# Kernel tuning notes

Measured on AMD Instinct MI355X. Metric: run time of the kernel, lower is better.

## Reference

```python
import jax, jax.numpy as jnp
import numpy as np

T, B, D, H = 2048, 4, 1024, 16
DK = D // H
SCALE = 1.0 / np.sqrt(DK)


def setup_inputs() -> dict:
    key = jax.random.key(0)
    k1, k2, k3 = jax.random.split(key, 3)
    x = jax.random.normal(k1, (T, B, D), dtype=jnp.float32)
    # xavier_uniform-ish scaling
    W_qkv = jax.random.normal(k2, (3 * D, D), dtype=jnp.float32) * np.sqrt(2.0 / (D + 3 * D))
    W_out = jax.random.normal(k3, (D, D), dtype=jnp.float32) * np.sqrt(1.0 / D)
    b_out = jnp.zeros((D,), dtype=jnp.float32)
    return {"x": x, "W_qkv": W_qkv, "W_out": W_out, "b_out": b_out}


def reference(x, W_qkv, W_out, b_out):
    Tn, Bn, Dn = x.shape
    # QKV projection (Linear with weight [3D, D], no bias)
    qkv = x @ W_qkv.T                                  # (T, B, 3D)
    qkv = qkv.reshape(Tn, Bn, 3, H, DK)
    q, k, v = qkv[:, :, 0], qkv[:, :, 1], qkv[:, :, 2]  # each (T, B, H, dk)
    scores = jnp.einsum('tbhd,sbhd->bhts', q, k) * SCALE  # (B, H, T, T)
    causal = jnp.triu(jnp.ones((Tn, Tn), dtype=bool), k=1)
    scores = jnp.where(causal, -jnp.inf, scores)
    attn = jax.nn.softmax(scores, axis=-1)
    out = jnp.einsum('bhts,sbhd->tbhd', attn, v)        # (T, B, H, dk)
    out = out.reshape(Tn, Bn, Dn)
    return out @ W_out.T + b_out
```

## Files before the change

### kernel.cpp

```cpp
#include <hip/hip_runtime.h>
#include <stdint.h>

#define T_DIM 2048
#define B_DIM 4
#define D_DIM 1024
#define H_NUM 16
#define HD 64
#define MROWS (T_DIM * B_DIM)
#define QKV_N (3 * D_DIM)
#define ATT_C 0.18033688011112042f

typedef unsigned short u16;
typedef __bf16 bf16x8 __attribute__((ext_vector_type(8)));
typedef float f32x4 __attribute__((ext_vector_type(4)));
typedef float f32x16 __attribute__((ext_vector_type(16)));
typedef u16 u16x4 __attribute__((ext_vector_type(4)));
typedef u16 u16x8 __attribute__((ext_vector_type(8)));

__device__ __forceinline__ u16 f2bf(float f) {
  union { float f; unsigned u; } v; v.f = f;
  unsigned r = v.u + 0x7fffu + ((v.u >> 16) & 1u);
  return (u16)(r >> 16);
}

__device__ __forceinline__ void async_copy16(void* lds, const void* g) {
  __builtin_amdgcn_global_load_lds((__attribute__((address_space(1))) void*)(g),
                                   (__attribute__((address_space(3))) void*)(lds),
                                   16, 0, 0);
}

__global__ __launch_bounds__(256) void cast3_f32_bf16(
    const float* __restrict__ s0, const float* __restrict__ s1,
    const float* __restrict__ s2, u16* __restrict__ dst,
    int n0, int n01, int ntot4) {
  int i = blockIdx.x * 256 + threadIdx.x;
  if (i >= ntot4) return;
  int e = i * 4;
  const float* s; int off;
  if (e < n0) { s = s0; off = 0; }
  else if (e < n01) { s = s1; off = n0; }
  else { s = s2; off = n01; }
  float4 v = *reinterpret_cast<const float4*>(s + (e - off));
  u16x4 o = {f2bf(v.x), f2bf(v.y), f2bf(v.z), f2bf(v.w)};
  *reinterpret_cast<u16x4*>(dst + e) = o;
}

template <int OUT_F32_BIAS>
__global__ __launch_bounds__(512, 1) void gemm_bt8b(
    const u16* __restrict__ A, const u16* __restrict__ Bm,
    u16* __restrict__ Cb, float* __restrict__ Cf, const float* __restrict__ bias,
    int M, int N, int K) {
  extern __shared__ u16 sm[];

  const int tid = threadIdx.x;
  const int lane = tid & 63, wid = tid >> 6;
  const int wr = wid >> 2, wc = wid & 3;
  const int l15 = lane & 15, lg = lane >> 4;
  const int xr = ((l15 >> 2) & 1) << 4;

  const int nwg = gridDim.x * gridDim.y;
  const int lin = blockIdx.y * gridDim.x + blockIdx.x;
  const int swz = (lin & 7) * (nwg >> 3) + (lin >> 3);
  const int bx = swz % gridDim.x, by = swz / gridDim.x;
  const int m0 = by * 128, n0 = bx * 256;

  const int srow = tid >> 3;
  const int kxs = ((tid & 7) * 8) ^ (((tid >> 5) & 1) << 4);
  const u16* gA = A + (size_t)(m0 + srow) * K + kxs;
  const u16* gB = Bm + (size_t)(n0 + srow) * K + kxs;

#define STGA(tk_, c_)                                                           \
  {                                                                             \
    _Pragma("unroll") for (int p = 0; p < 2; ++p)                               \
      async_copy16(sm + (c_) * 24576 + p * 4096 + tid * 8,                      \
                   gA + (size_t)(p * 64) * K + (size_t)(tk_) * 64);             \
  }
#define STGB(tk_, c_)                                                           \
  {                                                                             \
    _Pragma("unroll") for (int p = 0; p < 4; ++p)                               \
      async_copy16(sm + (c_) * 24576 + 8192 + p * 4096 + tid * 8,               \
                   gB + (size_t)(p * 64) * K + (size_t)(tk_) * 64);             \
  }
#define LDA_(mt_, kk_, c_)                                                      \
  (*reinterpret_cast<const bf16x8*>(sm + (c_) * 24576 +                         \
      (wr * 64 + (mt_) * 16 + l15) * 64 + (((kk_) * 32 + lg * 8) ^ xr)))
#define LDB_(nt_, kk_, c_)                                                      \
  (*reinterpret_cast<const bf16x8*>(sm + (c_) * 24576 + 8192 +                  \
      (wc * 64 + (nt_) * 16 + l15) * 64 + (((kk_) * 32 + lg * 8) ^ xr)))

  f32x4 acc[4][4];
#pragma unroll
  for (int i = 0; i < 4; i++)
#pragma unroll
    for (int j = 0; j < 4; j++) acc[i][j] = (f32x4){0.f, 0.f, 0.f, 0.f};

  const int NT = K >> 6;

  STGA(0, 0) STGB(0, 0) STGA(1, 1)
  asm volatile("s_waitcnt vmcnt(2)" ::: "memory");
  __builtin_amdgcn_sched_barrier(0);
  __builtin_amdgcn_s_barrier();

  for (int t = 0; t < NT; ++t) {
    const int c = t & 1;
    bf16x8 a03[4][2], b01[2][2], b23[2][2];
#pragma unroll
    for (int mt = 0; mt < 4; ++mt) {
      a03[mt][0] = LDA_(mt, 0, c);
      a03[mt][1] = LDA_(mt, 1, c);
    }
#pragma unroll
    for (int nt = 0; nt < 2; ++nt) {
      b01[nt][0] = LDB_(nt, 0, c);
      b01[nt][1] = LDB_(nt, 1, c);
    }
    if (t + 1 < NT) STGB(t + 1, c ^ 1)
    __builtin_amdgcn_s_barrier();
    asm volatile("s_waitcnt lgkmcnt(0)" ::: "memory");
    __builtin_amdgcn_sched_barrier(0);
    __builtin_amdgcn_s_setprio(1);
#pragma unroll
    for (int mt = 0; mt < 4; ++mt)
#pragma unroll
      for (int nt = 0; nt < 2; ++nt)
#pragma unroll
        for (int kk = 0; kk < 2; ++kk)
          acc[mt][nt] = __builtin_amdgcn_mfma_f32_16x16x32_bf16(
              a03[mt][kk], b01[nt][kk], acc[mt][nt], 0, 0, 0);
    __builtin_amdgcn_s_setprio(0);
    __builtin_amdgcn_s_barrier();
#pragma unroll
    for (int nt = 0; nt < 2; ++nt) {
      b23[nt][0] = LDB_(nt + 2, 0, c);
      b23[nt][1] = LDB_(nt + 2, 1, c);
    }
    if (t + 2 < NT) STGA(t + 2, c)
    __builtin_amdgcn_s_barrier();
    asm volatile("s_waitcnt lgkmcnt(0)" ::: "memory");
    __builtin_amdgcn_sched_barrier(0);
    __builtin_amdgcn_s_setprio(1);
#pragma unroll
    for (int mt = 0; mt < 4; ++mt)
#pragma unroll
      for (int nt = 0; nt < 2; ++nt)
#pragma unroll
        for (int kk = 0; kk < 2; ++kk)
          acc[mt][nt + 2] = __builtin_amdgcn_mfma_f32_16x16x32_bf16(
              a03[mt][kk], b23[nt][kk], acc[mt][nt + 2], 0, 0, 0);
    __builtin_amdgcn_s_setprio(0);
    if (t + 1 < NT) {
      if (t + 2 < NT) {
        asm volatile("s_waitcnt vmcnt(2)" ::: "memory");
      } else {
        asm volatile("s_waitcnt vmcnt(0)" ::: "memory");
      }
      __builtin_amdgcn_sched_barrier(0);
    }
    __builtin_amdgcn_s_barrier();
  }

  const float qsc = (!OUT_F32_BIAS && n0 < D_DIM) ? ATT_C : 1.0f;
#pragma unroll
  for (int mt = 0; mt < 4; ++mt) {
#pragma unroll
    for (int r = 0; r < 4; ++r) {
      const int row = m0 + wr * 64 + mt * 16 + lg * 4 + r;
#pragma unroll
      for (int nt = 0; nt < 4; ++nt) {
        const int col = n0 + wc * 64 + nt * 16 + l15;
        if (OUT_F32_BIAS) {
          Cf[(size_t)row * N + col] = acc[mt][nt][r] + bias[col];
        } else {
          Cb[(size_t)row * N + col] = f2bf(acc[mt][nt][r] * qsc);
        }
      }
    }
  }
#undef STGA
#undef STGB
#undef LDA_
#undef LDB_
}

#define VF_STRIDE 24
#define VF_FRAG (32 * VF_STRIDE)

__device__ __forceinline__ void process32(
    const bf16x8 (&qf)[4], f32x16 (&o)[2], f32x16& lacc,
    int q0w, int kv0, int l31, int hi, bool needMask, const bf16x8 onesf,
    const u16* __restrict__ Ks, const u16* __restrict__ Vf) {
  f32x16 s[2];
#pragma unroll
  for (int kb = 0; kb < 2; ++kb)
#pragma unroll
    for (int r = 0; r < 16; ++r) s[kb][r] = 0.f;

  __builtin_amdgcn_s_setprio(1);
#pragma unroll
  for (int kb = 0; kb < 2; ++kb) {
#pragma unroll
    for (int ks = 0; ks < 4; ++ks) {
      const int row = kb * 32 + l31;
      bf16x8 kf = *reinterpret_cast<const bf16x8*>(
          &Ks[row * 64 + ((((ks << 1) | hi)) ^ (l31 & 7)) * 8]);
      s[kb] = __builtin_amdgcn_mfma_f32_32x32x16_bf16(kf, qf[ks], s[kb], 0, 0, 0);
    }
  }
  __builtin_amdgcn_s_setprio(0);

  if (needMask) {
    const int q = q0w + l31;
#pragma unroll
    for (int kb = 0; kb < 2; ++kb)
#pragma unroll
      for (int r = 0; r < 16; ++r) {
        const int kv = kv0 + kb * 32 + (r & 3) + ((r >> 2) << 3) + (hi << 2);
        if (kv > q) s[kb][r] = -1e30f;
      }
  }
#pragma unroll
  for (int kb = 0; kb < 2; ++kb)
#pragma unroll
    for (int r = 0; r < 16; ++r)
      s[kb][r] = __builtin_amdgcn_exp2f(s[kb][r]);

  union Frag { unsigned u[4]; bf16x8 v; };
  Frag pf[4];
#pragma unroll
  for (int kb = 0; kb < 2; ++kb)
#pragma unroll
    for (int g = 0; g < 2; ++g) {
#pragma unroll
      for (int t2 = 0; t2 < 2; ++t2) {
        unsigned x, y;
        asm("v_cvt_pk_bf16_f32 %0, %1, %2"
            : "=v"(x) : "v"(s[kb][g * 8 + t2 * 2]), "v"(s[kb][g * 8 + t2 * 2 + 1]));
        asm("v_cvt_pk_bf16_f32 %0, %1, %2"
            : "=v"(y) : "v"(s[kb][g * 8 + t2 * 2 + 4]), "v"(s[kb][g * 8 + t2 * 2 + 5]));
        asm("v_permlane32_swap_b32 %0, %1" : "+v"(x), "+v"(y));
        pf[kb * 2 + g].u[t2] = x;
        pf[kb * 2 + g].u[t2 + 2] = y;
      }
    }

  __builtin_amdgcn_s_setprio(1);
#pragma unroll
  for (int ks = 0; ks < 4; ++ks) {
    lacc = __builtin_amdgcn_mfma_f32_32x32x16_bf16(onesf, pf[ks].v, lacc, 0, 0, 0);
#pragma unroll
    for (int db = 0; db < 2; ++db) {
      bf16x8 vf = *reinterpret_cast<const bf16x8*>(
          &Vf[(ks * 2 + db) * VF_FRAG + l31 * VF_STRIDE + hi * 8]);
      o[db] = __builtin_amdgcn_mfma_f32_32x32x16_bf16(vf, pf[ks].v, o[db], 0, 0, 0);
    }
  }
  __builtin_amdgcn_s_setprio(0);
}

__global__ __launch_bounds__(256, 2) void attn_kernel(
    const u16* __restrict__ qkv, u16* __restrict__ aout) {
  __shared__ __attribute__((aligned(16))) u16 Ks[128 * 64];
  __shared__ __attribute__((aligned(16))) u16 Vf[16 * VF_FRAG];

  const int tid = threadIdx.x;
  const int lane = tid & 63, w = tid >> 6;
  const int l31 = lane & 31, hi = lane >> 5;

  const int nwg = gridDim.x * gridDim.y;
  const int lin = blockIdx.y * gridDim.x + blockIdx.x;
  const int swz = (lin & 7) * (nwg >> 3) + (lin >> 3);
  const int px = swz % gridDim.x;
  const int bh = swz / gridDim.x;
  const int b = bh >> 4, h = bh & 15;
  const int qtA = px, qtB = 15 - px;
  const int q0A = qtA * 128 + w * 32, q0B = qtB * 128 + w * 32;

  bf16x8 qfA[4], qfB[4];
  {
    const u16* pA = qkv + ((size_t)(q0A + l31) * B_DIM + b) * QKV_N + h * HD + hi * 8;
    const u16* pB = qkv + ((size_t)(q0B + l31) * B_DIM + b) * QKV_N + h * HD + hi * 8;
#pragma unroll
    for (int ks = 0; ks < 4; ++ks) {
      qfA[ks] = *reinterpret_cast<const bf16x8*>(pA + ks * 16);
      qfB[ks] = *reinterpret_cast<const bf16x8*>(pB + ks * 16);
    }
  }

  bf16x8 onesf;
  {
    union { u16 u[8]; bf16x8 v; } ou;
#pragma unroll
    for (int i = 0; i < 8; ++i) ou.u[i] = 0x3F80;
    onesf = ou.v;
  }

  f32x16 oA[2], oB[2], laccA, laccB;
#pragma unroll
  for (int r = 0; r < 16; ++r) { laccA[r] = 0.f; laccB[r] = 0.f; }
#pragma unroll
  for (int db = 0; db < 2; ++db)
#pragma unroll
    for (int r = 0; r < 16; ++r) { oA[db][r] = 0.f; oB[db][r] = 0.f; }

  const int srow = tid >> 3;
  const int scol = (tid & 7) * 8;
  const int csw = (tid & 7) ^ (srow & 7);

  for (int kt2 = 0; kt2 <= qtB; ++kt2) {
    const int base = kt2 * 128;
#pragma unroll
    for (int p = 0; p < 4; ++p) {
      const u16* gK = qkv + ((size_t)(base + p * 32 + srow) * B_DIM + b) * QKV_N +
                      D_DIM + h * HD + csw * 8;
      async_copy16(Ks + tid * 8 + p * 2048, gK);
    }
    u16x8 vv[4];
#pragma unroll
    for (int p = 0; p < 4; ++p) {
      const u16* gV = qkv + ((size_t)(base + p * 32 + srow) * B_DIM + b) * QKV_N +
                      2 * D_DIM + h * HD + scol;
      vv[p] = *reinterpret_cast<const u16x8*>(gV);
    }
#pragma unroll
    for (int p = 0; p < 4; ++p) {
      const int kvl = p * 32 + srow;
      const int fb = (kvl >> 4) * 2;
      const int e16 = kvl & 15;
#pragma unroll
      for (int jj = 0; jj < 8; ++jj) {
        const int j = (jj + srow) & 7;
        const int d = scol + j;
        Vf[(fb + (d >> 5)) * VF_FRAG + (d & 31) * VF_STRIDE + e16] = vv[p][j];
      }
    }
    __syncthreads();

#pragma unroll
    for (int half = 0; half < 2; ++half) {
      const int kv0 = base + half * 64;
      const u16* Kh = Ks + half * (64 * 64);
      const u16* Vh = Vf + half * 8 * VF_FRAG;
      if (kv0 <= q0A + 31)
        process32(qfA, oA, laccA, q0A, kv0, l31, hi, kv0 + 63 > q0A, onesf, Kh, Vh);
      if (kv0 <= q0B + 31)
        process32(qfB, oB, laccB, q0B, kv0, l31, hi, kv0 + 63 > q0B, onesf, Kh, Vh);
    }
    __syncthreads();
  }

#pragma unroll
  for (int t = 0; t < 2; ++t) {
    const float inv = 1.0f / (t == 0 ? laccA[0] : laccB[0]);
    const int q0w = t == 0 ? q0A : q0B;
    f32x16* o = t == 0 ? oA : oB;
    u16* orow = aout + ((size_t)(q0w + l31) * B_DIM + b) * D_DIM + h * HD;
#pragma unroll
    for (int db = 0; db < 2; ++db)
#pragma unroll
      for (int rq = 0; rq < 4; ++rq) {
        u16x4 o4;
#pragma unroll
        for (int e = 0; e < 4; ++e) o4[e] = f2bf(o[db][rq * 4 + e] * inv);
        *reinterpret_cast<u16x4*>(orow + db * 32 + rq * 8 + hi * 4) = o4;
      }
  }
}

extern "C" void kernel_launch(void* const* d_in, const int* in_sizes, int n_in,
                              void* d_out, int out_size, void* d_ws, size_t ws_size,
                              hipStream_t stream) {
  (void)in_sizes; (void)n_in; (void)out_size; (void)ws_size;
  const float* x = (const float*)d_in[0];
  const float* Wqkv = (const float*)d_in[1];
  const float* Wout = (const float*)d_in[2];
  const float* bout = (const float*)d_in[3];
  float* out = (float*)d_out;

  u16* xb = (u16*)d_ws;
  u16* wqkvb = xb + (size_t)MROWS * D_DIM;
  u16* woutb = wqkvb + (size_t)QKV_N * D_DIM;
  u16* qkv = woutb + (size_t)D_DIM * D_DIM;
  u16* aout = qkv + (size_t)MROWS * QKV_N;

  {
    const int n0 = MROWS * D_DIM;
    const int n01 = n0 + QKV_N * D_DIM;
    const int ntot = n01 + D_DIM * D_DIM;
    const int n4 = ntot / 4;
    cast3_f32_bf16<<<(n4 + 255) / 256, 256, 0, stream>>>(
        x, Wqkv, Wout, xb, n0, n01, n4);
  }

  hipFuncSetAttribute((const void*)gemm_bt8b<0>,
                      hipFuncAttributeMaxDynamicSharedMemorySize, 98304);
  gemm_bt8b<0><<<dim3(QKV_N / 256, MROWS / 128), 512, 98304, stream>>>(
      xb, wqkvb, qkv, nullptr, nullptr, MROWS, QKV_N, D_DIM);

  attn_kernel<<<dim3(8, B_DIM * H_NUM), 256, 0, stream>>>(qkv, aout);

  hipFuncSetAttribute((const void*)gemm_bt8b<1>,
                      hipFuncAttributeMaxDynamicSharedMemorySize, 98304);
  gemm_bt8b<1><<<dim3(D_DIM / 256, MROWS / 128), 512, 98304, stream>>>(
      aout, woutb, nullptr, out, bout, MROWS, D_DIM, D_DIM);
}
```

Before: 178.5 us.

## Load V tiles via async global-to-LDS copy and read with transposing LDS loads

V tiles were loaded into registers and scattered element-by-element into a padded transposed LDS layout. Now they are copied straight to LDS with async global_load_lds in a blocked layout, and the MFMA operands are formed with ds_read_b64_tr_b16 transposing reads. This removes the register round trip and many 2-byte LDS stores per tile. In exchange it inserts a full lgkmcnt(0) wait and a sched_barrier before each set of PV MFMAs, which can serialize LDS latency with compute.

New measurement: 158.7 us, median of 2. 11.1% less time.

```diff
diff --git a/kernel.cpp b/kernel.cpp
--- a/kernel.cpp
+++ b/kernel.cpp
@@ -16,6 +16,7 @@
 typedef float f32x16 __attribute__((ext_vector_type(16)));
 typedef u16 u16x4 __attribute__((ext_vector_type(4)));
 typedef u16 u16x8 __attribute__((ext_vector_type(8)));
+typedef unsigned u32x2 __attribute__((ext_vector_type(2)));
 
 __device__ __forceinline__ u16 f2bf(float f) {
   union { float f; unsigned u; } v; v.f = f;
@@ -182,13 +183,11 @@
 #undef LDB_
 }
 
-#define VF_STRIDE 24
-#define VF_FRAG (32 * VF_STRIDE)
 
 __device__ __forceinline__ void process32(
     const bf16x8 (&qf)[4], f32x16 (&o)[2], f32x16& lacc,
     int q0w, int kv0, int l31, int hi, bool needMask, const bf16x8 onesf,
-    const u16* __restrict__ Ks, const u16* __restrict__ Vf) {
+    const u16* __restrict__ Ks, unsigned vh_lane) {
   f32x16 s[2];
 #pragma unroll
   for (int kb = 0; kb < 2; ++kb)
@@ -243,24 +242,31 @@
       }
     }
 
-  __builtin_amdgcn_s_setprio(1);
 #pragma unroll
   for (int ks = 0; ks < 4; ++ks) {
+    u32x2 t00, t01, t10, t11;
+    const unsigned a = vh_lane + ks * 2048;
+    asm volatile("ds_read_b64_tr_b16 %0, %1" : "=v"(t00) : "v"(a) : "memory");
+    asm volatile("ds_read_b64_tr_b16 %0, %1 offset:512" : "=v"(t01) : "v"(a) : "memory");
+    asm volatile("ds_read_b64_tr_b16 %0, %1 offset:256" : "=v"(t10) : "v"(a) : "memory");
+    asm volatile("ds_read_b64_tr_b16 %0, %1 offset:768" : "=v"(t11) : "v"(a) : "memory");
+    asm volatile("s_waitcnt lgkmcnt(0)" ::: "memory");
+    __builtin_amdgcn_sched_barrier(0);
+    union VF { u32x2 h2[2]; bf16x8 v; } u0, u1;
+    u0.h2[0] = t00; u0.h2[1] = t01;
+    u1.h2[0] = t10; u1.h2[1] = t11;
+    __builtin_amdgcn_s_setprio(1);
     lacc = __builtin_amdgcn_mfma_f32_32x32x16_bf16(onesf, pf[ks].v, lacc, 0, 0, 0);
-#pragma unroll
-    for (int db = 0; db < 2; ++db) {
-      bf16x8 vf = *reinterpret_cast<const bf16x8*>(
-          &Vf[(ks * 2 + db) * VF_FRAG + l31 * VF_STRIDE + hi * 8]);
-      o[db] = __builtin_amdgcn_mfma_f32_32x32x16_bf16(vf, pf[ks].v, o[db], 0, 0, 0);
-    }
-  }
-  __builtin_amdgcn_s_setprio(0);
+    o[0] = __builtin_amdgcn_mfma_f32_32x32x16_bf16(u0.v, pf[ks].v, o[0], 0, 0, 0);
+    o[1] = __builtin_amdgcn_mfma_f32_32x32x16_bf16(u1.v, pf[ks].v, o[1], 0, 0, 0);
+    __builtin_amdgcn_s_setprio(0);
+  }
 }
 
 __global__ __launch_bounds__(256, 2) void attn_kernel(
     const u16* __restrict__ qkv, u16* __restrict__ aout) {
   __shared__ __attribute__((aligned(16))) u16 Ks[128 * 64];
-  __shared__ __attribute__((aligned(16))) u16 Vf[16 * VF_FRAG];
+  __shared__ __attribute__((aligned(16))) u16 Vs[8192];
 
   const int tid = threadIdx.x;
   const int lane = tid & 63, w = tid >> 6;
@@ -303,8 +309,22 @@
     for (int r = 0; r < 16; ++r) { oA[db][r] = 0.f; oB[db][r] = 0.f; }
 
   const int srow = tid >> 3;
-  const int scol = (tid & 7) * 8;
   const int csw = (tid & 7) ^ (srow & 7);
+
+  int rowoffV[4], dcolV[4];
+#pragma unroll
+  for (int p = 0; p < 4; ++p) {
+    const int x0 = tid * 8 + p * 2048;
+    const int halfv = x0 >> 12, xh = x0 & 4095;
+    const int s = xh >> 6, r = (xh >> 4) & 3, c0 = xh & 15;
+    rowoffV[p] = halfv * 64 + (s >> 2) * 4 + r;
+    dcolV[p] = (s & 3) * 16 + c0;
+  }
+
+  const unsigned vlane = (unsigned)(lane >> 5) * 1024u +
+                         (unsigned)((lane >> 4) & 1) * 128u +
+                         (unsigned)(lane & 15) * 8u;
+  const unsigned vs0 = (unsigned)(uintptr_t)&Vs[0];
 
   for (int kt2 = 0; kt2 <= qtB; ++kt2) {
     const int base = kt2 * 128;
@@ -314,24 +334,11 @@
                       D_DIM + h * HD + csw * 8;
       async_copy16(Ks + tid * 8 + p * 2048, gK);
     }
-    u16x8 vv[4];
 #pragma unroll
     for (int p = 0; p < 4; ++p) {
-      const u16* gV = qkv + ((size_t)(base + p * 32 + srow) * B_DIM + b) * QKV_N +
-                      2 * D_DIM + h * HD + scol;
-      vv[p] = *reinterpret_cast<const u16x8*>(gV);
-    }
-#pragma unroll
-    for (int p = 0; p < 4; ++p) {
-      const int kvl = p * 32 + srow;
-      const int fb = (kvl >> 4) * 2;
-      const int e16 = kvl & 15;
-#pragma unroll
-      for (int jj = 0; jj < 8; ++jj) {
-        const int j = (jj + srow) & 7;
-        const int d = scol + j;
-        Vf[(fb + (d >> 5)) * VF_FRAG + (d & 31) * VF_STRIDE + e16] = vv[p][j];
-      }
+      const u16* gV = qkv + ((size_t)(base + rowoffV[p]) * B_DIM + b) * QKV_N +
+                      2 * D_DIM + h * HD + dcolV[p];
+      async_copy16(Vs + tid * 8 + p * 2048, gV);
     }
     __syncthreads();
 
@@ -339,11 +346,11 @@
     for (int half = 0; half < 2; ++half) {
       const int kv0 = base + half * 64;
       const u16* Kh = Ks + half * (64 * 64);
-      const u16* Vh = Vf + half * 8 * VF_FRAG;
+      const unsigned vh_lane = vs0 + half * 8192 + vlane;
       if (kv0 <= q0A + 31)
-        process32(qfA, oA, laccA, q0A, kv0, l31, hi, kv0 + 63 > q0A, onesf, Kh, Vh);
+        process32(qfA, oA, laccA, q0A, kv0, l31, hi, kv0 + 63 > q0A, onesf, Kh, vh_lane);
       if (kv0 <= q0B + 31)
-        process32(qfB, oB, laccB, q0B, kv0, l31, hi, kv0 + 63 > q0B, onesf, Kh, Vh);
+        process32(qfB, oB, laccB, q0B, kv0, l31, hi, kv0 + 63 > q0B, onesf, Kh, vh_lane);
     }
     __syncthreads();
   }
```
